# Optimization experiments

Measured on AMD Instinct MI355X. Metric: run time of the kernel, lower is better.

## Reference

```python
import jax, jax.numpy as jnp
import numpy as np

IN_SIZE = 1024
HID = 2048
OUT = 1024
M_STEPS = 100   # max extra ponder steps -> up to M_STEPS+1 total steps
EPS = 0.01


def setup_inputs() -> dict:
    key = jax.random.key(0)
    ks = jax.random.split(key, 11)
    inv = 1.0 / np.sqrt(HID)

    def unif(k, shape, scale):
        return jax.random.uniform(k, shape, jnp.float32, -scale, scale)

    return {
        "x": jax.random.normal(ks[0], (IN_SIZE,), jnp.float32),
        "h0": jax.random.normal(ks[1], (HID,), jnp.float32) * 0.1,
        "c0": jax.random.normal(ks[2], (HID,), jnp.float32) * 0.1,
        "W_ih": unif(ks[3], (4 * HID, 1 + IN_SIZE), inv),
        "b_ih": unif(ks[4], (4 * HID,), inv),
        "W_hh": unif(ks[5], (4 * HID, HID), inv),
        "b_hh": unif(ks[6], (4 * HID,), inv),
        "w_halt": unif(ks[7], (HID,), inv),
        "b_halt": jnp.ones((1,), jnp.float32),  # fc_halt.bias = 1.0 per source
        "W_out": unif(ks[8], (OUT, HID), inv),
        "b_out": unif(ks[9], (OUT,), inv),
    }


def reference(x, h0, c0, W_ih, b_ih, W_hh, b_hh, w_halt, b_halt, W_out, b_out):
    # Input contribution is constant across steps except the prepended halt flag
    # (1 on first step, 0 after). Precompute it once.
    ih_x = W_ih[:, 1:] @ x + b_ih + b_hh      # (4H,)
    w_flag = W_ih[:, 0]                        # (4H,)

    def step(carry, flag):
        h, c = carry
        gates = ih_x + flag * w_flag + W_hh @ h  # (4H,)
        i, f, g, o = jnp.split(gates, 4)
        i = jax.nn.sigmoid(i)
        f = jax.nn.sigmoid(f)
        g = jnp.tanh(g)
        o = jax.nn.sigmoid(o)
        c = f * c + i * g
        h = o * jnp.tanh(c)
        return (h, c), (h, c)

    flags = jnp.concatenate(
        [jnp.ones((1,), x.dtype), jnp.zeros((M_STEPS,), x.dtype)])
    _, (H, C) = jax.lax.scan(step, (h0, c0), flags)  # (M+1, HID) each

    p = jax.nn.sigmoid(H @ w_halt + b_halt[0])       # (M+1,) halting probs
    csum = jnp.cumsum(p)
    halted = csum >= 1.0 - EPS
    # n = first step where cumulative halt prob crosses threshold, capped at M
    n = jnp.where(jnp.any(halted), jnp.argmax(halted), M_STEPS)
    # remainder r = 1 - sum(p[:n]); csum[n] - p[n] == sum(p[:n])
    r = 1.0 - jnp.where(n > 0, csum[n] - p[n], 0.0)

    idx = jnp.arange(M_STEPS + 1)
    w = jnp.where(idx < n, p, jnp.where(idx == n, r, 0.0))  # (M+1,)

    outputs = H @ W_out.T + b_out                    # (M+1, OUT)
    output = w @ outputs                             # (OUT,) weights sum to 1
    h_out = w @ H                                    # (HID,)
    c_out = w @ C                                    # (HID,)
    ponder = n.astype(x.dtype) + 1.0 + r
    return output, (h_out, c_out), ponder
```

## Files before the change

### kernel.cpp

```cpp
#include <hip/hip_runtime.h>


#define HID    2048
#define INS    1024
#define OUTS   1024
#define MSTEPS 100
#define NBLK   256
#define NTHR   512
#define NWAVE  8
#define JPB    8
#define RPB    32
#define SLOTF  16

typedef unsigned long long u64;

#define KEEP4(v) asm volatile("" : "+v"((v).x), "+v"((v).y), "+v"((v).z), "+v"((v).w))

__device__ __forceinline__ float wave_reduce(float v) {
    #pragma unroll
    for (int off = 32; off > 0; off >>= 1)
        v += __shfl_down(v, off, 64);
    return v;
}

__device__ __forceinline__ u64 pack_tag(unsigned tag, float v) {
    return ((u64)tag << 32) | (u64)__float_as_uint(v);
}
__device__ __forceinline__ u64 aload(const u64* p) {
    return __hip_atomic_load(p, __ATOMIC_RELAXED, __HIP_MEMORY_SCOPE_AGENT);
}
__device__ __forceinline__ void astore(u64* p, u64 v) {
    __hip_atomic_store(p, v, __ATOMIC_RELAXED, __HIP_MEMORY_SCOPE_AGENT);
}


__global__ __launch_bounds__(NTHR, 2) void alstm_kernel(
    const float* __restrict__ x,      const float* __restrict__ h0,
    const float* __restrict__ c0,     const float* __restrict__ W_ih,
    const float* __restrict__ b_ih,   const float* __restrict__ W_hh,
    const float* __restrict__ b_hh,   const float* __restrict__ w_halt,
    const float* __restrict__ b_halt, const float* __restrict__ W_out,
    const float* __restrict__ b_out,  float* __restrict__ out,
    float* __restrict__ ws)
{
    const int b    = blockIdx.x;
    const int tid  = threadIdx.x;
    const int wave = tid >> 6;
    const int lane = tid & 63;

    float* arrive = ws;
    float* mail   = ws + NBLK * SLOTF;
    float* hbuf0  = ws + 2 * NBLK * SLOTF;
    float* hbuf1  = hbuf0 + HID;
    float* hbar_g = hbuf0 + 2 * HID;

    __shared__ float h_lds[HID];
    __shared__ float x_lds[INS];
    __shared__ float gate_lds[RPB];
    __shared__ float ihx_lds[RPB];
    __shared__ float wflag_lds[RPB];
    __shared__ float red_lds[4];
    __shared__ float bcast_lds;
    __shared__ float psum[NWAVE];

    const float bh = b_halt[0];
    const int j_own = b * JPB + tid;

    const int lr0 = 4 * wave;
    const int rbase = (lr0 >> 3) * HID + b * JPB + (lr0 & 7);

    #define SYNC_ROUND(tag_, part_, dot_) do {                                 \
        if (tid == 0) {                                                        \
            __threadfence();           \
            astore((u64*)(arrive + SLOTF * b), pack_tag((tag_), (part_)));     \
        }                                                                      \
        if (b == 0) {                                                          \
            float pf = 0.f;                                                    \
            if (tid < NBLK) {                                                  \
                u64 v;                                                         \
                do { v = aload((u64*)(arrive + SLOTF * tid)); }                \
                while ((unsigned)(v >> 32) != (unsigned)(tag_));               \
                pf = __uint_as_float((unsigned)v);                             \
            }                                                                  \
            float s = wave_reduce(pf);                                         \
            if (lane == 0 && wave < 4) red_lds[wave] = s;                      \
            __syncthreads();                                                   \
            if (tid == 0)                                                      \
                bcast_lds = red_lds[0] + red_lds[1] + red_lds[2] + red_lds[3]; \
            __syncthreads();                                                   \
            if (tid < NBLK)                                                    \
                astore((u64*)(mail + SLOTF * tid), pack_tag((tag_), bcast_lds)); \
        }                                                                      \
        if (tid == 0) {                                                        \
            u64 v;                                                             \
            do { v = aload((u64*)(mail + SLOTF * b)); }                        \
            while ((unsigned)(v >> 32) != (unsigned)(tag_));                   \
            bcast_lds = __uint_as_float((unsigned)v);                          \
            __threadfence();        \
        }                                                                      \
        __syncthreads();                                                       \
        (dot_) = bcast_lds;                                                    \
    } while (0)

    float4 w0r[8], w1r[8], w2r[8], w3r[8];
    {
        const float4* p0 = (const float4*)(W_hh + (size_t)rbase * HID);
        const float4* p1 = (const float4*)(W_hh + (size_t)(rbase + 1) * HID);
        const float4* p2 = (const float4*)(W_hh + (size_t)(rbase + 2) * HID);
        const float4* p3 = (const float4*)(W_hh + (size_t)(rbase + 3) * HID);
        #pragma unroll
        for (int m = 0; m < 8; ++m) {
            w0r[m] = p0[lane + 64 * m];
            w1r[m] = p1[lane + 64 * m];
            w2r[m] = p2[lane + 64 * m];
            w3r[m] = p3[lane + 64 * m];
        }
    }
    const int orow  = b * 4 + (wave & 3);
    const int ohalf = wave >> 2;
    float4 wor[4];
    {
        const float4* po = (const float4*)(W_out + (size_t)orow * HID) + ohalf * 256;
        #pragma unroll
        for (int m = 0; m < 4; ++m) wor[m] = po[lane + 64 * m];
    }

    ((float2*)x_lds)[tid] = ((const float2*)x)[tid];
    ((float4*)h_lds)[tid] = ((const float4*)h0)[tid];
    __syncthreads();

    #pragma unroll
    for (int rr = 0; rr < 4; ++rr) {
        const int lr = lr0 + rr;
        const int r  = (lr >> 3) * HID + b * JPB + (lr & 7);
        const float* wrow = W_ih + (size_t)r * (INS + 1) + 1;
        const int mis = (r + 1) & 3;
        const int p0  = (4 - mis) & 3;
        const int nv  = (INS - p0) >> 2;
        const float4* wv = (const float4*)(wrow + p0);
        float acc = 0.f;
        for (int i = lane; i < nv; i += 64) {
            float4 w4 = wv[i];
            int k = p0 + 4 * i;
            acc += w4.x * x_lds[k] + w4.y * x_lds[k + 1]
                 + w4.z * x_lds[k + 2] + w4.w * x_lds[k + 3];
        }
        if (lane == 0) {
            for (int k = 0; k < p0; ++k)            acc += wrow[k] * x_lds[k];
            for (int k = p0 + 4 * nv; k < INS; ++k) acc += wrow[k] * x_lds[k];
        }
        acc = wave_reduce(acc);
        if (lane == 0) {
            ihx_lds[lr]   = acc + b_ih[r] + b_hh[r];
            wflag_lds[lr] = W_ih[(size_t)r * (INS + 1)];
        }
    }

    #pragma unroll
    for (int m = 0; m < 8; ++m) {
        KEEP4(w0r[m]); KEEP4(w1r[m]); KEEP4(w2r[m]); KEEP4(w3r[m]);
    }
    #pragma unroll
    for (int m = 0; m < 4; ++m) KEEP4(wor[m]);

    float c_reg = 0.f, h_reg = 0.f, hbar = 0.f, cbar = 0.f;
    if (tid < JPB) c_reg = c0[j_own];

    float csum = 0.f, r_halt = 0.f;
    int   n_halt = 0;
    for (int t = 0; t <= MSTEPS; ++t) {
        {
            const float4* hv = (const float4*)h_lds;
            float a0 = 0.f, a1 = 0.f, a2 = 0.f, a3 = 0.f;
            #pragma unroll
            for (int m = 0; m < 8; ++m) {
                float4 hh = hv[lane + 64 * m];
                a0 += w0r[m].x * hh.x + w0r[m].y * hh.y + w0r[m].z * hh.z + w0r[m].w * hh.w;
                a1 += w1r[m].x * hh.x + w1r[m].y * hh.y + w1r[m].z * hh.z + w1r[m].w * hh.w;
                a2 += w2r[m].x * hh.x + w2r[m].y * hh.y + w2r[m].z * hh.z + w2r[m].w * hh.w;
                a3 += w3r[m].x * hh.x + w3r[m].y * hh.y + w3r[m].z * hh.z + w3r[m].w * hh.w;
            }
            a0 = wave_reduce(a0);
            a1 = wave_reduce(a1);
            a2 = wave_reduce(a2);
            a3 = wave_reduce(a3);
            if (lane == 0) {
                float bb0 = ihx_lds[lr0 + 0], bb1 = ihx_lds[lr0 + 1];
                float bb2 = ihx_lds[lr0 + 2], bb3 = ihx_lds[lr0 + 3];
                if (t == 0) {
                    bb0 += wflag_lds[lr0 + 0]; bb1 += wflag_lds[lr0 + 1];
                    bb2 += wflag_lds[lr0 + 2]; bb3 += wflag_lds[lr0 + 3];
                }
                gate_lds[lr0 + 0] = bb0 + a0;
                gate_lds[lr0 + 1] = bb1 + a1;
                gate_lds[lr0 + 2] = bb2 + a2;
                gate_lds[lr0 + 3] = bb3 + a3;
            }
        }
        __syncthreads();

        float part = 0.f;
        float* hdst = (t & 1) ? hbuf1 : hbuf0;
        if (tid < JPB) {
            float iv = gate_lds[0 * JPB + tid];
            float fv = gate_lds[1 * JPB + tid];
            float gv = gate_lds[2 * JPB + tid];
            float ov = gate_lds[3 * JPB + tid];
            iv = 1.f / (1.f + expf(-iv));
            fv = 1.f / (1.f + expf(-fv));
            gv = tanhf(gv);
            ov = 1.f / (1.f + expf(-ov));
            c_reg = fv * c_reg + iv * gv;
            h_reg = ov * tanhf(c_reg);
            hdst[j_own] = h_reg;
            part = h_reg * w_halt[j_own];
        }
        part += __shfl_down(part, 4, 64);
        part += __shfl_down(part, 2, 64);
        part += __shfl_down(part, 1, 64);

        float dotv;
        SYNC_ROUND(t + 1, part, dotv);

        float p = 1.f / (1.f + expf(-(dotv + bh)));
        float prev = csum;
        csum += p;
        bool halt_now = (csum >= 1.f - 0.01f) || (t == MSTEPS);
        float wt = halt_now ? (1.f - prev) : p;
        if (tid < JPB) { hbar += wt * h_reg; cbar += wt * c_reg; }
        if (halt_now) { n_halt = t; r_halt = 1.f - prev; break; }

        __syncthreads();
        ((float4*)h_lds)[tid] = ((const float4*)hdst)[tid];
        __syncthreads();
    }

    if (tid < JPB) {
        out[OUTS + j_own]       = hbar;
        out[OUTS + HID + j_own] = cbar;
        hbar_g[j_own] = hbar;
    }
    if (b == 0 && tid == 0) out[OUTS + 2 * HID] = (float)(n_halt + 1) + r_halt;

    float dummy;
    SYNC_ROUND(n_halt + 2, 0.f, dummy);
    (void)dummy;

    __syncthreads();
    ((float4*)h_lds)[tid] = ((const float4*)hbar_g)[tid];
    __syncthreads();

    {
        const float4* hv = (const float4*)h_lds + ohalf * 256;
        float acc = 0.f;
        #pragma unroll
        for (int m = 0; m < 4; ++m) {
            float4 h4 = hv[lane + 64 * m];
            acc += wor[m].x * h4.x + wor[m].y * h4.y
                 + wor[m].z * h4.z + wor[m].w * h4.w;
        }
        acc = wave_reduce(acc);
        if (lane == 0) psum[wave] = acc;
    }
    __syncthreads();
    if (tid < 4) {
        int row = b * 4 + tid;
        out[row] = psum[tid] + psum[tid + 4] + b_out[row];
    }
    #undef SYNC_ROUND
}

extern "C" void kernel_launch(void* const* d_in, const int* in_sizes, int n_in,
                              void* d_out, int out_size, void* d_ws, size_t ws_size,
                              hipStream_t stream) {
    const float* x      = (const float*)d_in[0];
    const float* h0     = (const float*)d_in[1];
    const float* c0     = (const float*)d_in[2];
    const float* W_ih   = (const float*)d_in[3];
    const float* b_ih   = (const float*)d_in[4];
    const float* W_hh   = (const float*)d_in[5];
    const float* b_hh   = (const float*)d_in[6];
    const float* w_halt = (const float*)d_in[7];
    const float* b_halt = (const float*)d_in[8];
    const float* W_out  = (const float*)d_in[9];
    const float* b_out  = (const float*)d_in[10];
    float* out = (float*)d_out;
    float* ws  = (float*)d_ws;

    hipMemsetAsync(d_ws, 0, 32768, stream);

    alstm_kernel<<<dim3(NBLK), dim3(NTHR), 0, stream>>>(
        x, h0, c0, W_ih, b_ih, W_hh, b_hh, w_halt, b_halt, W_out, b_out,
        out, ws);
}
```

Measured before the change: 181.4 us.

## Stage W_hh and hidden state as bf16 in LDS instead of registers

The recurrent weight slice per block is converted to bf16 and kept in shared memory instead of being pinned in fp32 registers, and the hidden state is broadcast as packed bf16. W_out is now loaded from global memory after the loop instead of being held in registers. The aim is to cut register pressure and halve the bytes read per step. In exchange every step re-reads about 128KB of LDS and unpacks bf16, and the lower precision in the recurrence may shift the halting step.

Result: no change. 181.4 us (+0.0%).

```diff
diff --git a/kernel.cpp b/kernel.cpp
--- a/kernel.cpp
+++ b/kernel.cpp
@@ -13,8 +13,7 @@
 #define SLOTF  16
 
 typedef unsigned long long u64;
-
-#define KEEP4(v) asm volatile("" : "+v"((v).x), "+v"((v).y), "+v"((v).z), "+v"((v).w))
+typedef unsigned int u32;
 
 __device__ __forceinline__ float wave_reduce(float v) {
     #pragma unroll
@@ -23,6 +22,15 @@
     return v;
 }
 
+__device__ __forceinline__ u32 bf16_2(float a, float b) {
+    u32 ua = __float_as_uint(a), ub = __float_as_uint(b);
+    ua = (ua + 0x7fffu + ((ua >> 16) & 1u)) >> 16;
+    ub = (ub + 0x7fffu + ((ub >> 16) & 1u)) >> 16;
+    return ua | (ub << 16);
+}
+__device__ __forceinline__ float blo(u32 u) { return __uint_as_float(u << 16); }
+__device__ __forceinline__ float bhi(u32 u) { return __uint_as_float(u & 0xffff0000u); }
+
 __device__ __forceinline__ u64 pack_tag(unsigned tag, float v) {
     return ((u64)tag << 32) | (u64)__float_as_uint(v);
 }
@@ -34,7 +42,7 @@
 }
 
 
-__global__ __launch_bounds__(NTHR, 2) void alstm_kernel(
+__global__ __launch_bounds__(NTHR) void alstm_kernel(
     const float* __restrict__ x,      const float* __restrict__ h0,
     const float* __restrict__ c0,     const float* __restrict__ W_ih,
     const float* __restrict__ b_ih,   const float* __restrict__ W_hh,
@@ -54,8 +62,10 @@
     float* hbuf1  = hbuf0 + HID;
     float* hbar_g = hbuf0 + 2 * HID;
 
-    __shared__ float h_lds[HID];
+    __shared__ u32   whh_u[RPB * 1024];
+    __shared__ u32   hpk[HID / 2];
     __shared__ float x_lds[INS];
+    __shared__ float hbar_lds[HID];
     __shared__ float gate_lds[RPB];
     __shared__ float ihx_lds[RPB];
     __shared__ float wflag_lds[RPB];
@@ -66,7 +76,7 @@
     const float bh = b_halt[0];
     const int j_own = b * JPB + tid;
 
-    const int lr0 = 4 * wave;
+    const int lr0   = 4 * wave;
     const int rbase = (lr0 >> 3) * HID + b * JPB + (lr0 & 7);
 
     #define SYNC_ROUND(tag_, part_, dot_) do {                                 \
@@ -102,31 +112,23 @@
         (dot_) = bcast_lds;                                                    \
     } while (0)
 
-    float4 w0r[8], w1r[8], w2r[8], w3r[8];
+    ((float2*)x_lds)[tid] = ((const float2*)x)[tid];
     {
-        const float4* p0 = (const float4*)(W_hh + (size_t)rbase * HID);
-        const float4* p1 = (const float4*)(W_hh + (size_t)(rbase + 1) * HID);
-        const float4* p2 = (const float4*)(W_hh + (size_t)(rbase + 2) * HID);
-        const float4* p3 = (const float4*)(W_hh + (size_t)(rbase + 3) * HID);
+        float4 v = ((const float4*)h0)[tid];
+        hpk[2 * tid]     = bf16_2(v.x, v.y);
+        hpk[2 * tid + 1] = bf16_2(v.z, v.w);
+    }
+    #pragma unroll
+    for (int rr = 0; rr < 4; ++rr) {
+        const float4* src = (const float4*)(W_hh + (size_t)(rbase + rr) * HID);
+        u32* dst = whh_u + (lr0 + rr) * (HID / 2);
         #pragma unroll
         for (int m = 0; m < 8; ++m) {
-            w0r[m] = p0[lane + 64 * m];
-            w1r[m] = p1[lane + 64 * m];
-            w2r[m] = p2[lane + 64 * m];
-            w3r[m] = p3[lane + 64 * m];
-        }
-    }
-    const int orow  = b * 4 + (wave & 3);
-    const int ohalf = wave >> 2;
-    float4 wor[4];
-    {
-        const float4* po = (const float4*)(W_out + (size_t)orow * HID) + ohalf * 256;
-        #pragma unroll
-        for (int m = 0; m < 4; ++m) wor[m] = po[lane + 64 * m];
-    }
-
-    ((float2*)x_lds)[tid] = ((const float2*)x)[tid];
-    ((float4*)h_lds)[tid] = ((const float4*)h0)[tid];
+            float4 v = src[lane + 64 * m];
+            dst[2 * (lane + 64 * m)]     = bf16_2(v.x, v.y);
+            dst[2 * (lane + 64 * m) + 1] = bf16_2(v.z, v.w);
+        }
+    }
     __syncthreads();
 
     #pragma unroll
@@ -156,13 +158,6 @@
         }
     }
 
-    #pragma unroll
-    for (int m = 0; m < 8; ++m) {
-        KEEP4(w0r[m]); KEEP4(w1r[m]); KEEP4(w2r[m]); KEEP4(w3r[m]);
-    }
-    #pragma unroll
-    for (int m = 0; m < 4; ++m) KEEP4(wor[m]);
-
     float c_reg = 0.f, h_reg = 0.f, hbar = 0.f, cbar = 0.f;
     if (tid < JPB) c_reg = c0[j_own];
 
@@ -170,15 +165,28 @@
     int   n_halt = 0;
     for (int t = 0; t <= MSTEPS; ++t) {
         {
-            const float4* hv = (const float4*)h_lds;
+            const uint4* hp = (const uint4*)hpk;
             float a0 = 0.f, a1 = 0.f, a2 = 0.f, a3 = 0.f;
             #pragma unroll
-            for (int m = 0; m < 8; ++m) {
-                float4 hh = hv[lane + 64 * m];
-                a0 += w0r[m].x * hh.x + w0r[m].y * hh.y + w0r[m].z * hh.z + w0r[m].w * hh.w;
-                a1 += w1r[m].x * hh.x + w1r[m].y * hh.y + w1r[m].z * hh.z + w1r[m].w * hh.w;
-                a2 += w2r[m].x * hh.x + w2r[m].y * hh.y + w2r[m].z * hh.z + w2r[m].w * hh.w;
-                a3 += w3r[m].x * hh.x + w3r[m].y * hh.y + w3r[m].z * hh.z + w3r[m].w * hh.w;
+            for (int m = 0; m < 4; ++m) {
+                uint4 hu = hp[lane + 64 * m];
+                float h0a = blo(hu.x), h1a = bhi(hu.x);
+                float h2a = blo(hu.y), h3a = bhi(hu.y);
+                float h4a = blo(hu.z), h5a = bhi(hu.z);
+                float h6a = blo(hu.w), h7a = bhi(hu.w);
+                #pragma unroll
+                for (int rr = 0; rr < 4; ++rr) {
+                    const uint4* wp = (const uint4*)(whh_u + (lr0 + rr) * (HID / 2));
+                    uint4 wu = wp[lane + 64 * m];
+                    float s = blo(wu.x) * h0a + bhi(wu.x) * h1a
+                            + blo(wu.y) * h2a + bhi(wu.y) * h3a
+                            + blo(wu.z) * h4a + bhi(wu.z) * h5a
+                            + blo(wu.w) * h6a + bhi(wu.w) * h7a;
+                    if      (rr == 0) a0 += s;
+                    else if (rr == 1) a1 += s;
+                    else if (rr == 2) a2 += s;
+                    else              a3 += s;
+                }
             }
             a0 = wave_reduce(a0);
             a1 = wave_reduce(a1);
@@ -230,8 +238,11 @@
         if (tid < JPB) { hbar += wt * h_reg; cbar += wt * c_reg; }
         if (halt_now) { n_halt = t; r_halt = 1.f - prev; break; }
 
-        __syncthreads();
-        ((float4*)h_lds)[tid] = ((const float4*)hdst)[tid];
+        {
+            float4 v = ((const float4*)hdst)[tid];
+            hpk[2 * tid]     = bf16_2(v.x, v.y);
+            hpk[2 * tid + 1] = bf16_2(v.z, v.w);
+        }
         __syncthreads();
     }
 
@@ -247,17 +258,20 @@
     (void)dummy;
 
     __syncthreads();
-    ((float4*)h_lds)[tid] = ((const float4*)hbar_g)[tid];
+    ((float4*)hbar_lds)[tid] = ((const float4*)hbar_g)[tid];
     __syncthreads();
 
     {
-        const float4* hv = (const float4*)h_lds + ohalf * 256;
+        const int row  = b * 4 + (wave & 3);
+        const int half = wave >> 2;
+        const float4* wrow = (const float4*)(W_out + (size_t)row * HID) + half * 256;
+        const float4* hv   = (const float4*)hbar_lds + half * 256;
         float acc = 0.f;
         #pragma unroll
         for (int m = 0; m < 4; ++m) {
+            float4 w4 = wrow[lane + 64 * m];
             float4 h4 = hv[lane + 64 * m];
-            acc += wor[m].x * h4.x + wor[m].y * h4.y
-                 + wor[m].z * h4.z + wor[m].w * h4.w;
+            acc += w4.x * h4.x + w4.y * h4.y + w4.z * h4.z + w4.w * h4.w;
         }
         acc = wave_reduce(acc);
         if (lane == 0) psum[wave] = acc;
```
